# Optimization experiments

Hardware: AMD Instinct MI355X
Metric: run time of the kernel (lower is better)

Reference implementation:

```python
import jax, jax.numpy as jnp
import numpy as np

WS = 16      # window_size
OWS = 24     # overlap_win_size = int(16*0.5) + 16
PAD = 4      # (OWS - WS) // 2
NH = 6       # num_heads
DIM = 192
MLP_HID = 384  # dim * mlp_ratio(2)
TABLE = (WS + OWS - 1) ** 2  # 1521


def _ln(x, g, b, eps=1e-5):
    m = x.mean(-1, keepdims=True)
    v = ((x - m) ** 2).mean(-1, keepdims=True)
    return (x - m) * jax.lax.rsqrt(v + eps) * g + b


def setup_inputs() -> dict:
    key = jax.random.key(0)
    ks = jax.random.split(key, 16)
    B, H, W, C = 1, 192, 192, DIM
    x = jax.random.normal(ks[0], (B, H * W, C), jnp.float32)
    rpi = jax.random.randint(ks[1], (WS * WS, OWS * OWS), 0, TABLE, dtype=jnp.int64)
    s = 0.02
    return {
        "x": x,
        "rpi": rpi,
        "h": H,
        "w": W,
        "norm1_g": jnp.ones((C,), jnp.float32),
        "norm1_b": jnp.zeros((C,), jnp.float32),
        "qkv_w": jax.random.normal(ks[2], (C, 3 * C), jnp.float32) * s,
        "qkv_b": jnp.zeros((3 * C,), jnp.float32),
        "rpb_table": jax.random.normal(ks[3], (TABLE, NH), jnp.float32) * s,
        "proj_w": jax.random.normal(ks[4], (C, C), jnp.float32) * s,
        "proj_b": jnp.zeros((C,), jnp.float32),
        "norm2_g": jnp.ones((C,), jnp.float32),
        "norm2_b": jnp.zeros((C,), jnp.float32),
        "fc1_w": jax.random.normal(ks[5], (C, MLP_HID), jnp.float32) * s,
        "fc1_b": jnp.zeros((MLP_HID,), jnp.float32),
        "fc2_w": jax.random.normal(ks[6], (MLP_HID, C), jnp.float32) * s,
        "fc2_b": jnp.zeros((C,), jnp.float32),
    }


def reference(x, rpi, h, w, norm1_g, norm1_b, qkv_w, qkv_b, rpb_table,
              proj_w, proj_b, norm2_g, norm2_b, fc1_w, fc1_b, fc2_w, fc2_b):
    B, L, C = x.shape
    d = C // NH
    scale = d ** -0.5
    nhw, nww = h // WS, w // WS
    nW = nhw * nww

    shortcut = x
    xn = _ln(x, norm1_g, norm1_b).reshape(B, h, w, C)
    qkv = xn @ qkv_w + qkv_b                       # (B, h, w, 3C)
    q, k, v = jnp.split(qkv, 3, axis=-1)

    # non-overlapping query windows: (B*nW, WS*WS, C)
    qw = q.reshape(B, nhw, WS, nww, WS, C).transpose(0, 1, 3, 2, 4, 5)
    qw = qw.reshape(B * nW, WS * WS, C)

    # overlapping key/value windows via padded gather (equiv. to nn.Unfold)
    ri = (jnp.arange(nhw) * WS)[:, None] + jnp.arange(OWS)[None, :]  # (nhw, OWS)
    ci = (jnp.arange(nww) * WS)[:, None] + jnp.arange(OWS)[None, :]  # (nww, OWS)

    def win(t):
        tp = jnp.pad(t, ((0, 0), (PAD, PAD), (PAD, PAD), (0, 0)))
        g = tp[:, ri[:, :, None, None], ci[None, None, :, :], :]     # (B,nhw,OWS,nww,OWS,C)
        return g.transpose(0, 1, 3, 2, 4, 5).reshape(B * nW, OWS * OWS, C)

    kw, vw = win(k), win(v)

    qh = qw.reshape(B * nW, WS * WS, NH, d).transpose(0, 2, 1, 3) * scale
    kh = kw.reshape(B * nW, OWS * OWS, NH, d).transpose(0, 2, 1, 3)
    vh = vw.reshape(B * nW, OWS * OWS, NH, d).transpose(0, 2, 1, 3)

    attn = jnp.einsum('bhqd,bhkd->bhqk', qh, kh)
    bias = rpb_table[rpi.reshape(-1)].reshape(WS * WS, OWS * OWS, NH)
    bias = bias.transpose(2, 0, 1)                 # (NH, nq, n)
    attn = jax.nn.softmax(attn + bias[None], axis=-1)
    out = jnp.einsum('bhqk,bhkd->bhqd', attn, vh)
    out = out.transpose(0, 2, 1, 3).reshape(B * nW, WS * WS, C)

    # window reverse
    xr = out.reshape(B, nhw, nww, WS, WS, C).transpose(0, 1, 3, 2, 4, 5)
    xr = xr.reshape(B, h * w, C)

    x2 = xr @ proj_w + proj_b + shortcut
    x3 = _ln(x2, norm2_g, norm2_b)
    mlp = jax.nn.gelu(x3 @ fc1_w + fc1_b, approximate=False) @ fc2_w + fc2_b
    return x2 + mlp
```

## Files before the change

kernel.cpp:

```cpp
#include <hip/hip_runtime.h>
#include <hip/hip_bf16.h>

#define NH 6
#define DIM 192
#define HW 192
#define M_TOK (HW*HW)
#define QSC 0.25503488f
#define L2E 1.4426950408889634f

typedef __attribute__((ext_vector_type(8))) __bf16 bf16x8;
typedef __attribute__((ext_vector_type(8))) short short8;
typedef __attribute__((ext_vector_type(4))) short s16x4;
typedef __attribute__((ext_vector_type(4))) float floatx4;

__device__ inline unsigned short f2bf(float f) {
    union { float f; unsigned int u; } v; v.f = f;
    unsigned int r = (v.u + 0x7FFFu + ((v.u >> 16) & 1u)) >> 16;
    return (unsigned short)r;
}
__device__ inline short f2bfh(float f) {
    __bf16 b = (__bf16)f;
    return __builtin_bit_cast(short, b);
}
__device__ inline float exp2fast(float x) {
#if __has_builtin(__builtin_amdgcn_exp2f)
    return __builtin_amdgcn_exp2f(x);
#else
    return exp2f(x);
#endif
}
__device__ inline floatx4 bf4f(s16x4 b) {
    floatx4 f;
    #pragma unroll
    for (int r = 0; r < 4; r++) {
        union { unsigned u; float f; } v;
        v.u = ((unsigned)(unsigned short)b[r]) << 16;
        f[r] = v.f;
    }
    return f;
}

__device__ inline floatx4 mfma16(short8 a, short8 b, floatx4 c) {
    return __builtin_amdgcn_mfma_f32_16x16x32_bf16(
        __builtin_bit_cast(bf16x8, a), __builtin_bit_cast(bf16x8, b), c, 0, 0, 0);
}

template <int OFF>
__device__ inline s16x4 tr16(unsigned addr) {
    s16x4 r;
    asm volatile("ds_read_b64_tr_b16 %0, %1 offset:%2"
                 : "=&v"(r) : "v"(addr), "i"(OFF));
    return r;
}
template <int OFF>
__device__ inline s16x4 tr16m(unsigned addr) {
    s16x4 r;
    asm volatile("ds_read_b64_tr_b16 %0, %1 offset:%2"
                 : "=&v"(r) : "v"(addr), "i"(OFF) : "memory");
    return r;
}
template <int N>
__device__ __forceinline__ void wait_lgkm() {
    asm volatile("s_waitcnt lgkmcnt(%0)" :: "i"(N) : "memory");
}
__device__ inline short8 cat8(s16x4 a, s16x4 b) {
    return __builtin_shufflevector(a, b, 0, 1, 2, 3, 4, 5, 6, 7);
}

__device__ __forceinline__ void gload16(const void* g, unsigned lds_off) {
    __builtin_amdgcn_global_load_lds(
        (const __attribute__((address_space(1))) unsigned int*)(uintptr_t)g,
        (__attribute__((address_space(3))) unsigned int*)(uintptr_t)lds_off,
        16, 0, 0);
}

__global__ __launch_bounds__(256) void prep_kernel(
    const float* __restrict__ qkvw, const float* __restrict__ projw,
    const float* __restrict__ fc1w, const float* __restrict__ fc2w,
    const int* __restrict__ rpi, const float* __restrict__ table,
    const float* __restrict__ x, const float* __restrict__ n1g,
    const float* __restrict__ n1b,
    unsigned short* __restrict__ wt_qkv, unsigned short* __restrict__ wt_proj,
    unsigned short* __restrict__ wt_fc1, unsigned short* __restrict__ wt_fc2,
    unsigned short* __restrict__ btf, unsigned short* __restrict__ xn) {
    int bid = blockIdx.x;
    if (bid < 1152) {
        int id = bid * 256 + threadIdx.x;
        if (id < 110592) {
            int n = id / 192, k = id - n * 192;
            wt_qkv[id] = f2bf(qkvw[k * 576 + n]);
        } else if (id < 147456) {
            int i = id - 110592;
            int n = i / 192, k = i - n * 192;
            wt_proj[i] = f2bf(projw[k * 192 + n]);
        } else if (id < 221184) {
            int i = id - 147456;
            int n = i / 192, k = i - n * 192;
            wt_fc1[i] = f2bf(fc1w[k * 384 + n]);
        } else {
            int i = id - 221184;
            int n = i / 384, k = i - n * 384;
            wt_fc2[i] = f2bf(fc2w[k * 192 + n]);
        }
    } else if (bid < 2016) {
        int id = (bid - 1152) * 256 + threadIdx.x;
        int lane = id & 63;
        int t = id >> 6;
        int kt = t % 36; t /= 36;
        int qt = t & 15; int hh = t >> 4;
        int k = kt * 16 + (lane & 15);
        int qb = qt * 16 + (lane >> 4) * 4;
        s16x4 v;
        #pragma unroll
        for (int r = 0; r < 4; r++)
            v[r] = f2bfh(table[rpi[(qb + r) * 576 + k] * NH + hh] * L2E);
        *(s16x4*)&btf[(size_t)id * 4] = v;
    } else {
        int row = (bid - 2016) * 4 + (threadIdx.x >> 6);
        int lane = threadIdx.x & 63;
        const float* r = x + (size_t)row * DIM;
        float x0 = r[lane], x1 = r[lane + 64], x2 = r[lane + 128];
        float s = x0 + x1 + x2;
        #pragma unroll
        for (int m = 32; m >= 1; m >>= 1) s += __shfl_xor(s, m);
        float mean = s * (1.f / 192.f);
        float d0 = x0 - mean, d1 = x1 - mean, d2 = x2 - mean;
        float v = d0 * d0 + d1 * d1 + d2 * d2;
        #pragma unroll
        for (int m = 32; m >= 1; m >>= 1) v += __shfl_xor(v, m);
        float rstd = rsqrtf(v * (1.f / 192.f) + 1e-5f);
        unsigned short* o = xn + (size_t)row * DIM;
        o[lane]       = f2bf(d0 * rstd * n1g[lane]       + n1b[lane]);
        o[lane + 64]  = f2bf(d1 * rstd * n1g[lane + 64]  + n1b[lane + 64]);
        o[lane + 128] = f2bf(d2 * rstd * n1g[lane + 128] + n1b[lane + 128]);
    }
}

template <int MODE, int KK>
__global__ __launch_bounds__(256, 4) void gemm_kernel(
    const unsigned short* __restrict__ A,
    const unsigned short* __restrict__ Wt,
    const float* __restrict__ bias,
    void* __restrict__ outp,
    int N) {
    __shared__ __align__(16) short sAB[19968];
    constexpr int STAGES = KK / 96;
    int tid = threadIdx.x;
    int w = tid >> 6, lane = tid & 63;
    int bm = blockIdx.x, bn = blockIdx.y;
    int lr = lane & 15, h = lane >> 4;
    floatx4 acc[2][4];
    #pragma unroll
    for (int i = 0; i < 2; i++)
        #pragma unroll
        for (int j = 0; j < 4; j++) acc[i][j] = (floatx4){0.f, 0.f, 0.f, 0.f};

    unsigned ldsbase = (unsigned)(uintptr_t)&sAB[0];

    for (int s = 0; s < STAGES; s++) {
        if (s) __syncthreads();
        for (int W = w; W < 39; W += 4) {
            int o = W * 1024 + lane * 16;
            const unsigned short* src;
            if (o < 26624) {
                int r = o / 208;
                int c = (o - r * 208) >> 4; c = c < 12 ? c : 11;
                src = &A[(size_t)(bm * 128 + r) * KK + s * 96 + c * 8];
            } else {
                int o2 = o - 26624;
                int r = o2 / 208;
                int c = (o2 - r * 208) >> 4; c = c < 12 ? c : 11;
                src = &Wt[(size_t)(bn * 64 + r) * KK + s * 96 + c * 8];
            }
            gload16(src, ldsbase + (unsigned)(W * 1024));
        }
        __syncthreads();
        #pragma unroll
        for (int kk = 0; kk < 3; kk++) {
            int kc = (kk * 4 + h) * 8;
            short8 a0 = *(const short8*)&sAB[(w * 32 + lr) * 104 + kc];
            short8 a1 = *(const short8*)&sAB[(w * 32 + 16 + lr) * 104 + kc];
            short8 b0 = *(const short8*)&sAB[13312 + (lr) * 104 + kc];
            short8 b1 = *(const short8*)&sAB[13312 + (16 + lr) * 104 + kc];
            short8 b2 = *(const short8*)&sAB[13312 + (32 + lr) * 104 + kc];
            short8 b3 = *(const short8*)&sAB[13312 + (48 + lr) * 104 + kc];
            acc[0][0] = mfma16(a0, b0, acc[0][0]);
            acc[0][1] = mfma16(a0, b1, acc[0][1]);
            acc[0][2] = mfma16(a0, b2, acc[0][2]);
            acc[0][3] = mfma16(a0, b3, acc[0][3]);
            acc[1][0] = mfma16(a1, b0, acc[1][0]);
            acc[1][1] = mfma16(a1, b1, acc[1][1]);
            acc[1][2] = mfma16(a1, b2, acc[1][2]);
            acc[1][3] = mfma16(a1, b3, acc[1][3]);
        }
    }

    int rowbase = bm * 128 + w * 32 + h * 4;
    int colbase = bn * 64;
    #pragma unroll
    for (int mi = 0; mi < 2; mi++) {
        #pragma unroll
        for (int ni = 0; ni < 4; ni++) {
            int c = colbase + ni * 16 + lr;
            float bv = bias[c];
            #pragma unroll
            for (int j = 0; j < 4; j++) {
                int r = rowbase + mi * 16 + j;
                float v = acc[mi][ni][j] + bv;
                if (MODE == 0) {
                    int part = c / 192;
                    int rem = c - part * 192;
                    int hd = rem >> 5, d = rem & 31;
                    if (part == 0) v *= QSC;
                    ((unsigned short*)outp)[((size_t)(part * 6 + hd) * M_TOK + r) * 32 + d] = f2bf(v);
                } else if (MODE == 2) {
                    size_t idx = (size_t)r * N + c;
                    float gl = 0.5f * v * (1.f + erff(v * 0.70710678118654752f));
                    ((unsigned short*)outp)[idx] = f2bf(gl);
                } else {
                    size_t idx = (size_t)r * N + c;
                    ((float*)outp)[idx] = v + ((float*)outp)[idx];
                }
            }
        }
    }
}

__global__ __launch_bounds__(256, 3) void projln_kernel(
    const unsigned short* __restrict__ A,
    const unsigned short* __restrict__ Wt,
    const float* __restrict__ bias,
    const float* __restrict__ res,
    const float* __restrict__ g2, const float* __restrict__ b2,
    float* __restrict__ x2out,
    unsigned short* __restrict__ xnout) {
    __shared__ __align__(16) short sAB[26624];
    int tid = threadIdx.x;
    int w = tid >> 6, lane = tid & 63;
    int bm = blockIdx.x;
    int lr = lane & 15, h = lane >> 4;
    floatx4 acc[12];
    #pragma unroll
    for (int ni = 0; ni < 12; ni++) acc[ni] = (floatx4){0.f, 0.f, 0.f, 0.f};

    unsigned ldsbase = (unsigned)(uintptr_t)&sAB[0];

    for (int s = 0; s < 2; s++) {
        if (s) __syncthreads();
        for (int W = w; W < 52; W += 4) {
            int o = W * 1024 + lane * 16;
            const unsigned short* src;
            if (o < 13312) {
                int r = o / 208;
                int c = (o - r * 208) >> 4; c = c < 12 ? c : 11;
                int col = s * 96 + c * 8;
                int hd = col >> 5, d = col & 31;
                src = &A[((size_t)hd * M_TOK + bm * 64 + r) * 32 + d];
            } else {
                int o2 = o - 13312;
                int r = o2 / 208;
                int c = (o2 - r * 208) >> 4; c = c < 12 ? c : 11;
                src = &Wt[(size_t)r * 192 + s * 96 + c * 8];
            }
            gload16(src, ldsbase + (unsigned)(W * 1024));
        }
        __syncthreads();
        #pragma unroll
        for (int kk = 0; kk < 3; kk++) {
            int kc = (kk * 4 + h) * 8;
            short8 a0 = *(const short8*)&sAB[(w * 16 + lr) * 104 + kc];
            #pragma unroll
            for (int ni = 0; ni < 12; ni++) {
                short8 bfr = *(const short8*)&sAB[6656 + (ni * 16 + lr) * 104 + kc];
                acc[ni] = mfma16(a0, bfr, acc[ni]);
            }
        }
    }

    int row0 = bm * 64 + w * 16 + h * 4;
    float s1[4] = {0.f, 0.f, 0.f, 0.f}, s2[4] = {0.f, 0.f, 0.f, 0.f};
    #pragma unroll
    for (int ni = 0; ni < 12; ni++) {
        int c = ni * 16 + lr;
        float bv = bias[c];
        #pragma unroll
        for (int j = 0; j < 4; j++) {
            size_t idx = (size_t)(row0 + j) * 192 + c;
            float v = acc[ni][j] + bv + res[idx];
            acc[ni][j] = v;
            s1[j] += v;
            s2[j] += v * v;
        }
    }
    #pragma unroll
    for (int mask = 1; mask <= 8; mask <<= 1) {
        #pragma unroll
        for (int j = 0; j < 4; j++) {
            s1[j] += __shfl_xor(s1[j], mask);
            s2[j] += __shfl_xor(s2[j], mask);
        }
    }
    float mean[4], rstd[4];
    #pragma unroll
    for (int j = 0; j < 4; j++) {
        mean[j] = s1[j] * (1.f / 192.f);
        float var = s2[j] * (1.f / 192.f) - mean[j] * mean[j];
        rstd[j] = rsqrtf(var + 1e-5f);
    }
    #pragma unroll
    for (int ni = 0; ni < 12; ni++) {
        int c = ni * 16 + lr;
        float gw = g2[c], bw = b2[c];
        #pragma unroll
        for (int j = 0; j < 4; j++) {
            size_t idx = (size_t)(row0 + j) * 192 + c;
            float v = acc[ni][j];
            x2out[idx] = v;
            xnout[idx] = f2bf((v - mean[j]) * rstd[j] * gw + bw);
        }
    }
}

__global__ __launch_bounds__(256, 3) void attn_mfma_kernel(
    const unsigned short* __restrict__ qkv,
    const unsigned short* __restrict__ btf,
    unsigned short* __restrict__ out) {
    __shared__ __align__(16) short sK[2][2304];
    __shared__ __align__(16) short sV[2][2048];
    __shared__ __align__(16) short sPt[4][4096];
    int win = blockIdx.x, head = blockIdx.y;
    int iy = win / 12, ix = win % 12;
    int tid = threadIdx.x;
    int w = tid >> 6, lane = tid & 63;
    int m = lane & 15, h = lane >> 4;

    const unsigned short* Qp = qkv + (size_t)head * M_TOK * 32;
    const unsigned short* Kp = qkv + (size_t)(6 + head) * M_TOK * 32;

    short8 qf[4];
    #pragma unroll
    for (int i = 0; i < 4; i++) {
        int wy = w * 4 + i;
        size_t tok = (size_t)(iy * 16 + wy) * HW + ix * 16 + m;
        qf[i] = *(const short8*)&Qp[tok * 32 + h * 8];
    }

    floatx4 oacc[4][2];
    floatx4 li4[4];
    #pragma unroll
    for (int i = 0; i < 4; i++) {
        li4[i] = (floatx4){0.f, 0.f, 0.f, 0.f};
        oacc[i][0] = (floatx4){0.f, 0.f, 0.f, 0.f};
        oacc[i][1] = (floatx4){0.f, 0.f, 0.f, 0.f};
    }

    int skey = tid >> 2, dq = tid & 3;
    short* kdst = &sK[0][skey * 36 + dq * 8];
    short* vdst = &sV[0][(dq >> 1) * 1024 + (skey >> 2) * 64 + (skey & 3) * 16 + (dq & 1) * 8];

    auto fetch = [&](int c, short8& kv, short8& vv) {
        int key = c * 64 + skey;
        int oy = key / 24, ox = key - (key / 24) * 24;
        int gy = iy * 16 - 4 + oy, gx = ix * 16 - 4 + ox;
        kv = (short8){0,0,0,0,0,0,0,0};
        vv = (short8){0,0,0,0,0,0,0,0};
        if (gy >= 0 && gy < HW && gx >= 0 && gx < HW) {
            const unsigned short* p = &Kp[((size_t)gy * HW + gx) * 32 + dq * 8];
            kv = *(const short8*)p;
            vv = *(const short8*)(p + 6 * M_TOK * 32);
        }
    };

    {
        short8 kv, vv;
        fetch(0, kv, vv);
        *(short8*)kdst = kv;
        *(short8*)vdst = vv;
    }

    unsigned sPbase = (unsigned)(uintptr_t)&sPt[w][0];
    unsigned sPa = sPbase + 8 * m + 256 * h;
    unsigned sVa0 = (unsigned)(uintptr_t)&sV[0][0] + 8 * m + 256 * h;
    char* sPwb = (char*)&sPt[w][0] + 128 * (m >> 2) + 32 * (m & 3) + 8 * h;

    for (int c = 0; c < 9; c++) {
        __syncthreads();
        int cur = c & 1;
        short8 knx, vnx;
        bool more = (c < 8);
        if (more) fetch(c + 1, knx, vnx);

        const short* sKc = sK[cur];
        short8 kfrag[4];
        #pragma unroll
        for (int kt = 0; kt < 4; kt++)
            kfrag[kt] = *(const short8*)&sKc[(kt * 16 + m) * 36 + h * 8];

        const unsigned short* bb = btf + ((((size_t)head * 16 + w * 4) * 36 + c * 4) * 64 + lane) * 4;

        #pragma unroll
        for (int i = 0; i < 4; i++) {
            floatx4 s[4];
            #pragma unroll
            for (int kt = 0; kt < 4; kt++)
                s[kt] = bf4f(*(const s16x4*)&bb[(size_t)(i * 36 + kt) * 256]);
            #pragma unroll
            for (int kt = 0; kt < 4; kt++)
                s[kt] = mfma16(qf[i], kfrag[kt], s[kt]);
            #pragma unroll
            for (int kt = 0; kt < 4; kt++) {
                s16x4 pk;
                #pragma unroll
                for (int r = 0; r < 4; r++)
                    pk[r] = f2bfh(exp2fast(s[kt][r]));
                *(s16x4*)(sPwb + i * 2048 + kt * 512) = pk;
                li4[i] += bf4f(pk);
            }
        }

        unsigned sVa = sVa0 + cur * 4096;
        short8 vb[4];
        {
            s16x4 lo0 = tr16<0>(sVa),    hi0 = tr16<128>(sVa);
            s16x4 lo1 = tr16<2048>(sVa), hi1 = tr16<2176>(sVa);
            s16x4 lo2 = tr16<1024>(sVa), hi2 = tr16<1152>(sVa);
            s16x4 lo3 = tr16<3072>(sVa), hi3 = tr16<3200>(sVa);
            vb[0] = cat8(lo0, hi0);
            vb[1] = cat8(lo1, hi1);
            vb[2] = cat8(lo2, hi2);
            vb[3] = cat8(lo3, hi3);
        }
        s16x4 pl0 = tr16m<0>(sPa),    ph0 = tr16m<128>(sPa);
        s16x4 pl1 = tr16m<1024>(sPa), ph1 = tr16m<1152>(sPa);
        #pragma unroll
        for (int i = 0; i < 4; i++) {
            s16x4 nl0, nh0, nl1, nh1;
            if (i < 3) {
                unsigned a = sPa + (unsigned)((i + 1) * 2048);
                nl0 = tr16m<0>(a);    nh0 = tr16m<128>(a);
                nl1 = tr16m<1024>(a); nh1 = tr16m<1152>(a);
                wait_lgkm<4>();
            } else {
                wait_lgkm<0>();
            }
            __builtin_amdgcn_sched_barrier(0);
            short8 pa0 = cat8(pl0, ph0);
            short8 pa1 = cat8(pl1, ph1);
            oacc[i][0] = mfma16(pa0, vb[0], oacc[i][0]);
            oacc[i][1] = mfma16(pa0, vb[1], oacc[i][1]);
            oacc[i][0] = mfma16(pa1, vb[2], oacc[i][0]);
            oacc[i][1] = mfma16(pa1, vb[3], oacc[i][1]);
            if (i < 3) { pl0 = nl0; ph0 = nh0; pl1 = nl1; ph1 = nh1; }
        }

        if (more) {
            int nb = 1 - cur;
            *(short8*)(kdst + nb * 2304) = knx;
            *(short8*)(vdst + nb * 2048) = vnx;
        }
    }

    #pragma unroll
    for (int i = 0; i < 4; i++) {
        #pragma unroll
        for (int mask = 1; mask <= 8; mask <<= 1) {
            li4[i][0] += __shfl_xor(li4[i][0], mask);
            li4[i][1] += __shfl_xor(li4[i][1], mask);
            li4[i][2] += __shfl_xor(li4[i][2], mask);
            li4[i][3] += __shfl_xor(li4[i][3], mask);
        }
    }

    unsigned short* Op = out + (size_t)head * M_TOK * 32;
    #pragma unroll
    for (int i = 0; i < 4; i++) {
        float inv[4];
        #pragma unroll
        for (int r = 0; r < 4; r++)
            inv[r] = 1.f / li4[i][r];
        int wy = w * 4 + i;
        #pragma unroll
        for (int dt = 0; dt < 2; dt++)
            #pragma unroll
            for (int r = 0; r < 4; r++) {
                size_t tok = (size_t)(iy * 16 + wy) * HW + ix * 16 + h * 4 + r;
                Op[tok * 32 + dt * 16 + m] = f2bf(oacc[i][dt][r] * inv[r]);
            }
    }
}

extern "C" void kernel_launch(void* const* d_in, const int* in_sizes, int n_in,
                              void* d_out, int out_size, void* d_ws, size_t ws_size,
                              hipStream_t stream) {
    const float* x     = (const float*)d_in[0];
    const int*   rpi   = (const int*)d_in[1];
    const float* n1g   = (const float*)d_in[4];
    const float* n1b   = (const float*)d_in[5];
    const float* qkvw  = (const float*)d_in[6];
    const float* qkvb  = (const float*)d_in[7];
    const float* rpb   = (const float*)d_in[8];
    const float* projw = (const float*)d_in[9];
    const float* projb = (const float*)d_in[10];
    const float* n2g   = (const float*)d_in[11];
    const float* n2b   = (const float*)d_in[12];
    const float* fc1w  = (const float*)d_in[13];
    const float* fc1b  = (const float*)d_in[14];
    const float* fc2w  = (const float*)d_in[15];
    const float* fc2b  = (const float*)d_in[16];

    char* ws = (char*)d_ws;
    unsigned short* wt_qkv  = (unsigned short*)ws;
    unsigned short* wt_proj = wt_qkv + 110592;
    unsigned short* wt_fc1  = wt_proj + 36864;
    unsigned short* wt_fc2  = wt_fc1 + 73728;
    unsigned short* btf     = (unsigned short*)(ws + 589824);
    unsigned short* xn      = (unsigned short*)(ws + 4128768);
    unsigned short* qkv     = (unsigned short*)(ws + 18284544);
    unsigned short* attn_o  = (unsigned short*)(ws + 60751872);

    prep_kernel<<<11232, 256, 0, stream>>>(qkvw, projw, fc1w, fc2w, rpi, rpb,
                                           x, n1g, n1b,
                                           wt_qkv, wt_proj, wt_fc1, wt_fc2,
                                           btf, xn);
    gemm_kernel<0, 192><<<dim3(288, 9), 256, 0, stream>>>(
        xn, wt_qkv, qkvb, qkv, 576);
    attn_mfma_kernel<<<dim3(144, 6), 256, 0, stream>>>(qkv, btf, attn_o);
    projln_kernel<<<576, 256, 0, stream>>>(
        attn_o, wt_proj, projb, x, n2g, n2b, (float*)d_out, xn);
    gemm_kernel<2, 192><<<dim3(288, 6), 256, 0, stream>>>(
        xn, wt_fc1, fc1b, qkv, 384);
    gemm_kernel<3, 384><<<dim3(288, 3), 256, 0, stream>>>(
        qkv, wt_fc2, fc2b, d_out, 192);
}
```

Baseline: 156.8 us.

## Interleave QK and PV stages with double-buffered P tile to raise occupancy

Restructures the per-chunk attention loop so the QK^T/exp stage of row-block i+1 is interleaved with the P·V MFMAs of row-block i. The P scratch buffer shrinks from four slots to two (ping-pong), and V fragments are transposed-read up front. LDS writes of P now go through inline-asm ds_write_b64, with explicit lgkmcnt waits and sched barriers. The smaller LDS footprint lets launch bounds rise to 4 blocks per SIMD. This aims to hide LDS latency and raise occupancy, but risks register pressure or spills under the tighter bound, and correctness now rests on hand-counted waits.

```diff
diff --git a/kernel.cpp b/kernel.cpp
--- a/kernel.cpp
+++ b/kernel.cpp
@@ -46,18 +46,16 @@
 }
 
 template <int OFF>
-__device__ inline s16x4 tr16(unsigned addr) {
-    s16x4 r;
-    asm volatile("ds_read_b64_tr_b16 %0, %1 offset:%2"
-                 : "=&v"(r) : "v"(addr), "i"(OFF));
-    return r;
-}
-template <int OFF>
 __device__ inline s16x4 tr16m(unsigned addr) {
     s16x4 r;
     asm volatile("ds_read_b64_tr_b16 %0, %1 offset:%2"
                  : "=&v"(r) : "v"(addr), "i"(OFF) : "memory");
     return r;
+}
+template <int OFF>
+__device__ __forceinline__ void dswr64(unsigned addr, s16x4 v) {
+    asm volatile("ds_write_b64 %0, %1 offset:%2"
+                 :: "v"(addr), "v"(v), "i"(OFF) : "memory");
 }
 template <int N>
 __device__ __forceinline__ void wait_lgkm() {
@@ -321,13 +319,13 @@
     }
 }
 
-__global__ __launch_bounds__(256, 3) void attn_mfma_kernel(
+__global__ __launch_bounds__(256, 4) void attn_mfma_kernel(
     const unsigned short* __restrict__ qkv,
     const unsigned short* __restrict__ btf,
     unsigned short* __restrict__ out) {
     __shared__ __align__(16) short sK[2][2304];
     __shared__ __align__(16) short sV[2][2048];
-    __shared__ __align__(16) short sPt[4][4096];
+    __shared__ __align__(16) short sPt[4][2048];
     int win = blockIdx.x, head = blockIdx.y;
     int iy = win / 12, ix = win % 12;
     int tid = threadIdx.x;
@@ -378,10 +376,37 @@
         *(short8*)vdst = vv;
     }
 
-    unsigned sPbase = (unsigned)(uintptr_t)&sPt[w][0];
-    unsigned sPa = sPbase + 8 * m + 256 * h;
+    unsigned sPa  = (unsigned)(uintptr_t)&sPt[w][0] + 8 * m + 256 * h;
+    unsigned sPwA = (unsigned)(uintptr_t)&sPt[w][0] + 128 * (m >> 2) + 32 * (m & 3) + 8 * h;
     unsigned sVa0 = (unsigned)(uintptr_t)&sV[0][0] + 8 * m + 256 * h;
-    char* sPwb = (char*)&sPt[w][0] + 128 * (m >> 2) + 32 * (m & 3) + 8 * h;
+
+#define DO_A(i) { \
+    floatx4 s_[4]; \
+    _Pragma("unroll") for (int kt = 0; kt < 4; kt++) \
+        s_[kt] = bf4f(*(const s16x4*)&bb[((i) * 36 + kt) * 256]); \
+    _Pragma("unroll") for (int kt = 0; kt < 4; kt++) \
+        s_[kt] = mfma16(qf[i], kfrag[kt], s_[kt]); \
+    unsigned wa_ = sPwA + (((i) & 1) << 11); \
+    _Pragma("unroll") for (int kt = 0; kt < 4; kt++) { \
+        s16x4 pk_; \
+        _Pragma("unroll") for (int r = 0; r < 4; r++) \
+            pk_[r] = f2bfh(exp2fast(s_[kt][r])); \
+        li4[i] += bf4f(pk_); \
+        if (kt == 0)      dswr64<0>(wa_, pk_); \
+        else if (kt == 1) dswr64<512>(wa_, pk_); \
+        else if (kt == 2) dswr64<1024>(wa_, pk_); \
+        else              dswr64<1536>(wa_, pk_); \
+    } }
+
+#define DO_PR(i, d) { unsigned ra_ = sPa + (((i) & 1) << 11); \
+    d##l0 = tr16m<0>(ra_);    d##h0 = tr16m<128>(ra_); \
+    d##l1 = tr16m<1024>(ra_); d##h1 = tr16m<1152>(ra_); }
+
+#define DO_B(i, d) { short8 pa0_ = cat8(d##l0, d##h0), pa1_ = cat8(d##l1, d##h1); \
+    oacc[i][0] = mfma16(pa0_, vb0, oacc[i][0]); \
+    oacc[i][1] = mfma16(pa0_, vb1, oacc[i][1]); \
+    oacc[i][0] = mfma16(pa1_, vb2, oacc[i][0]); \
+    oacc[i][1] = mfma16(pa1_, vb3, oacc[i][1]); }
 
     for (int c = 0; c < 9; c++) {
         __syncthreads();
@@ -395,63 +420,40 @@
         #pragma unroll
         for (int kt = 0; kt < 4; kt++)
             kfrag[kt] = *(const short8*)&sKc[(kt * 16 + m) * 36 + h * 8];
+        wait_lgkm<0>();
+        __builtin_amdgcn_sched_barrier(0);
+
+        unsigned sVa = sVa0 + cur * 4096;
+        s16x4 lo0 = tr16m<0>(sVa),    hi0 = tr16m<128>(sVa);
+        s16x4 lo1 = tr16m<2048>(sVa), hi1 = tr16m<2176>(sVa);
+        s16x4 lo2 = tr16m<1024>(sVa), hi2 = tr16m<1152>(sVa);
+        s16x4 lo3 = tr16m<3072>(sVa), hi3 = tr16m<3200>(sVa);
 
         const unsigned short* bb = btf + ((((size_t)head * 16 + w * 4) * 36 + c * 4) * 64 + lane) * 4;
 
-        #pragma unroll
-        for (int i = 0; i < 4; i++) {
-            floatx4 s[4];
-            #pragma unroll
-            for (int kt = 0; kt < 4; kt++)
-                s[kt] = bf4f(*(const s16x4*)&bb[(size_t)(i * 36 + kt) * 256]);
-            #pragma unroll
-            for (int kt = 0; kt < 4; kt++)
-                s[kt] = mfma16(qf[i], kfrag[kt], s[kt]);
-            #pragma unroll
-            for (int kt = 0; kt < 4; kt++) {
-                s16x4 pk;
-                #pragma unroll
-                for (int r = 0; r < 4; r++)
-                    pk[r] = f2bfh(exp2fast(s[kt][r]));
-                *(s16x4*)(sPwb + i * 2048 + kt * 512) = pk;
-                li4[i] += bf4f(pk);
-            }
-        }
-
-        unsigned sVa = sVa0 + cur * 4096;
-        short8 vb[4];
-        {
-            s16x4 lo0 = tr16<0>(sVa),    hi0 = tr16<128>(sVa);
-            s16x4 lo1 = tr16<2048>(sVa), hi1 = tr16<2176>(sVa);
-            s16x4 lo2 = tr16<1024>(sVa), hi2 = tr16<1152>(sVa);
-            s16x4 lo3 = tr16<3072>(sVa), hi3 = tr16<3200>(sVa);
-            vb[0] = cat8(lo0, hi0);
-            vb[1] = cat8(lo1, hi1);
-            vb[2] = cat8(lo2, hi2);
-            vb[3] = cat8(lo3, hi3);
-        }
-        s16x4 pl0 = tr16m<0>(sPa),    ph0 = tr16m<128>(sPa);
-        s16x4 pl1 = tr16m<1024>(sPa), ph1 = tr16m<1152>(sPa);
-        #pragma unroll
-        for (int i = 0; i < 4; i++) {
-            s16x4 nl0, nh0, nl1, nh1;
-            if (i < 3) {
-                unsigned a = sPa + (unsigned)((i + 1) * 2048);
-                nl0 = tr16m<0>(a);    nh0 = tr16m<128>(a);
-                nl1 = tr16m<1024>(a); nh1 = tr16m<1152>(a);
-                wait_lgkm<4>();
-            } else {
-                wait_lgkm<0>();
-            }
-            __builtin_amdgcn_sched_barrier(0);
-            short8 pa0 = cat8(pl0, ph0);
-            short8 pa1 = cat8(pl1, ph1);
-            oacc[i][0] = mfma16(pa0, vb[0], oacc[i][0]);
-            oacc[i][1] = mfma16(pa0, vb[1], oacc[i][1]);
-            oacc[i][0] = mfma16(pa1, vb[2], oacc[i][0]);
-            oacc[i][1] = mfma16(pa1, vb[3], oacc[i][1]);
-            if (i < 3) { pl0 = nl0; ph0 = nh0; pl1 = nl1; ph1 = nh1; }
-        }
+        s16x4 pAl0, pAh0, pAl1, pAh1, pBl0, pBh0, pBl1, pBh1;
+        DO_A(0);
+        DO_PR(0, pA);
+        DO_A(1);
+        DO_PR(1, pB);
+        wait_lgkm<8>();
+        __builtin_amdgcn_sched_barrier(0);
+        short8 vb0 = cat8(lo0, hi0), vb1 = cat8(lo1, hi1);
+        short8 vb2 = cat8(lo2, hi2), vb3 = cat8(lo3, hi3);
+        DO_B(0, pA);
+        DO_A(2);
+        DO_PR(2, pA);
+        wait_lgkm<8>();
+        __builtin_amdgcn_sched_barrier(0);
+        DO_B(1, pB);
+        DO_A(3);
+        DO_PR(3, pB);
+        wait_lgkm<8>();
+        __builtin_amdgcn_sched_barrier(0);
+        DO_B(2, pA);
+        wait_lgkm<0>();
+        __builtin_amdgcn_sched_barrier(0);
+        DO_B(3, pB);
 
         if (more) {
             int nb = 1 - cur;
@@ -459,6 +461,9 @@
             *(short8*)(vdst + nb * 2048) = vnx;
         }
     }
+#undef DO_A
+#undef DO_PR
+#undef DO_B
 
     #pragma unroll
     for (int i = 0; i < 4; i++) {
```

New measurement: 247.1 us. 1.58x slower.
